# Kernel optimization log

Measured on AMD Instinct MI355X. Metric: run time of the kernel, lower is better.

## Reference

```python
import jax, jax.numpy as jnp
import numpy as np

B, S, CL = 64, 250, 16
WV, CV, FV, LAB = 50000, 100, 10, 20
WD, CD, CH, FD, HD = 300, 300, 50, 5, 200
T = LAB + 2          # CRF lattice size (labels + START + STOP)
START, STOP = LAB, LAB + 1
H = HD // 2          # hidden per LSTM direction
IN = CH + WD + FD    # 355


def _lstm_dir(x, m, w_ih, w_hh, b):
    # x: [B,S,IN], m: [B,S] bool -> masked unidirectional LSTM (PyTorch gate order i,f,g,o)
    Bn = x.shape[0]
    def step(carry, inp):
        h, c = carry
        xt, mt = inp
        g = xt @ w_ih.T + h @ w_hh.T + b
        i, f, gg, o = jnp.split(g, 4, axis=-1)
        c_new = jax.nn.sigmoid(f) * c + jax.nn.sigmoid(i) * jnp.tanh(gg)
        h_new = jax.nn.sigmoid(o) * jnp.tanh(c_new)
        mt = mt[:, None]
        h = jnp.where(mt, h_new, h)
        c = jnp.where(mt, c_new, c)
        return (h, c), h
    init = (jnp.zeros((Bn, H), x.dtype), jnp.zeros((Bn, H), x.dtype))
    _, hs = jax.lax.scan(step, init, (x.transpose(1, 0, 2), m.T))
    return hs.transpose(1, 0, 2)  # [B,S,H]


def _viterbi(feats, mask, trans):
    # feats: [B,S,T], mask: [B,S] bool, trans: [T,T] (trans[i,j] = score i->j)
    Bn = feats.shape[0]
    delta0 = trans[START][None, :] + feats[:, 0]  # [B,T]
    ident = jnp.arange(T)[None, :]
    def step(delta, inp):
        f_t, m_t = inp                              # [B,T], [B]
        sc = delta[:, :, None] + trans[None]        # [B,T(prev),T(cur)]
        vmax = sc.max(axis=1)
        bp = sc.argmax(axis=1)                      # [B,T]
        m = m_t[:, None]
        delta = jnp.where(m, vmax + f_t, delta)
        bp = jnp.where(m, bp, ident)                # pads: pass-through pointer
        return delta, bp
    delta, bps = jax.lax.scan(step, delta0,
                              (feats[:, 1:].transpose(1, 0, 2), mask[:, 1:].T))
    final = delta + trans[:, STOP][None, :]
    score = final.max(axis=1)                       # [B]
    last = final.argmax(axis=1)                     # [B]
    ar = jnp.arange(Bn)
    def back(tag, bp):
        prev = bp[ar, tag]
        return prev, prev
    _, prevs = jax.lax.scan(back, last, bps, reverse=True)  # [S-1,B]
    tag_seq = jnp.concatenate([prevs.transpose(1, 0), last[:, None]], axis=1)  # [B,S]
    return score, tag_seq


def setup_inputs() -> dict:
    key = jax.random.key(0)
    ks = jax.random.split(key, 20)
    lens = jax.random.randint(ks[0], (B,), S // 2, S + 1)
    mask = (jnp.arange(S)[None, :] < lens[:, None])
    def u(k, shape, scale):
        return jax.random.uniform(k, shape, jnp.float32, -scale, scale)
    return {
        "batch_word": jax.random.randint(ks[1], (B, S), 0, WV),
        "batch_features": jax.random.randint(ks[2], (B, S), 0, FV),
        "batch_wordlen": lens,
        "batch_char": jax.random.randint(ks[3], (B * S, CL), 0, CV),
        "batch_charlen": jax.random.randint(ks[4], (B * S,), 1, CL + 1),
        "batch_charrecover": jnp.arange(B * S),
        "mask": mask,
        "char_emb": u(ks[5], (CV, CD), np.sqrt(3.0 / CD)),
        "word_emb": u(ks[6], (WV, WD), np.sqrt(3.0 / WD)),
        "feat_emb": u(ks[7], (FV, FD), np.sqrt(3.0 / FD)),
        "conv_w": 0.1 * jax.random.normal(ks[8], (CH, CD, 3), jnp.float32),
        "conv_b": jnp.zeros((CH,), jnp.float32),
        "w_ih_f": 0.1 * jax.random.normal(ks[9], (4 * H, IN), jnp.float32),
        "w_hh_f": 0.1 * jax.random.normal(ks[10], (4 * H, H), jnp.float32),
        "b_f": jnp.zeros((4 * H,), jnp.float32),
        "w_ih_b": 0.1 * jax.random.normal(ks[11], (4 * H, IN), jnp.float32),
        "w_hh_b": 0.1 * jax.random.normal(ks[12], (4 * H, H), jnp.float32),
        "b_b": jnp.zeros((4 * H,), jnp.float32),
        "proj_w": 0.1 * jax.random.normal(ks[13], (HD, T), jnp.float32),
        "proj_b": jnp.zeros((T,), jnp.float32),
        "trans": 0.1 * jax.random.normal(ks[14], (T, T), jnp.float32),
    }


def reference(batch_word, batch_features, batch_wordlen, batch_char, batch_charlen,
              batch_charrecover, mask, char_emb, word_emb, feat_emb, conv_w, conv_b,
              w_ih_f, w_hh_f, b_f, w_ih_b, w_hh_b, b_b, proj_w, proj_b, trans):
    # char CNN: embed -> conv1d(k=3, pad=1) -> global max-pool (dropout: eval mode, identity)
    ce = char_emb[batch_char]                          # [B*S, CL, CD]
    conv = jax.lax.conv_general_dilated(
        ce.transpose(0, 2, 1), conv_w, window_strides=(1,), padding=[(1, 1)],
        dimension_numbers=('NCH', 'OIH', 'NCH')) + conv_b[None, :, None]
    char_feat = conv.max(axis=2)                       # [B*S, CH]
    char_feat = char_feat[batch_charrecover].reshape(B, S, CH)
    word_rep = jnp.concatenate(
        [word_emb[batch_word], char_feat, feat_emb[batch_features]], axis=2)  # [B,S,IN]
    # masked BiLSTM (equivalent to pack_padded_sequence: pads never update state)
    h_f = _lstm_dir(word_rep, mask, w_ih_f, w_hh_f, b_f)
    h_b = _lstm_dir(word_rep[:, ::-1], mask[:, ::-1], w_ih_b, w_hh_b, b_b)[:, ::-1]
    lstm_out = jnp.concatenate([h_f, h_b], axis=2)     # [B,S,HD]
    feats = lstm_out @ proj_w + proj_b                 # [B,S,T]
    score, tag_seq = _viterbi(feats, mask, trans)
    return tag_seq
```

## Files before the change

### kernel.cpp

```cpp
#include <hip/hip_runtime.h>
#include <hip/hip_bf16.h>
#include <math.h>

#define WS_U        0
#define WS_WPAD     15360
#define WS_WREP     359424
#define WS_PRE      6503424
#define WS_LSTM     359424
#define WS_FEATS    3559424

__global__ __launch_bounds__(256) void prepw_kernel(
    const float* __restrict__ wf, const float* __restrict__ wb,
    float* __restrict__ w_pad) {
  int idx = blockIdx.x * 256 + threadIdx.x;
  if (idx >= 896 * 384) return;
  int col = idx % 384, row = idx / 384;
  float v = 0.f;
  if (col < 355) {
    if (row < 400)      v = wf[row * 355 + col];
    else if (row < 800) v = wb[(row - 400) * 355 + col];
  }
  w_pad[idx] = v;
}

__global__ __launch_bounds__(256) void u_kernel(
    const float* __restrict__ char_emb, const float* __restrict__ conv_w,
    float* __restrict__ U) {
  int idx = blockIdx.x * 256 + threadIdx.x;
  if (idx >= 15000) return;
  int c = idx / 150, rem = idx % 150, k = rem / 50, o = rem % 50;
  float acc = 0.f;
  for (int i = 0; i < 300; i++)
    acc += char_emb[c * 300 + i] * conv_w[(o * 300 + i) * 3 + k];
  U[idx] = acc;
}

__global__ __launch_bounds__(64) void assemble_kernel(
    const int* __restrict__ batch_word, const int* __restrict__ batch_feats,
    const int* __restrict__ batch_char, const int* __restrict__ recover,
    const float* __restrict__ word_emb, const float* __restrict__ feat_emb,
    const float* __restrict__ conv_b, const float* __restrict__ U,
    float* __restrict__ wrep) {
  int n = blockIdx.x;
  int tid = threadIdx.x;
  __shared__ int ch[16];
  if (tid < 16) ch[tid] = batch_char[(size_t)recover[n] * 16 + tid];
  __syncthreads();
  float* dst = wrep + (size_t)n * 384;
  int w = batch_word[n];
  for (int i = tid; i < 300; i += 64) dst[i] = word_emb[(size_t)w * 300 + i];
  if (tid < 34) {
    int i = 350 + tid;
    dst[i] = (i < 355) ? feat_emb[batch_feats[n] * 5 + (i - 350)] : 0.f;
  }
  if (tid < 50) {
    int o = tid;
    float bo = conv_b[o];
    float m = -1e30f;
#pragma unroll
    for (int l = 0; l < 16; l++) {
      float v = bo + U[(ch[l] * 3 + 1) * 50 + o];
      if (l > 0)  v += U[(ch[l - 1] * 3 + 0) * 50 + o];
      if (l < 15) v += U[(ch[l + 1] * 3 + 2) * 50 + o];
      m = fmaxf(m, v);
    }
    dst[300 + o] = m;
  }
}

__global__ __launch_bounds__(256, 4) void gemm_kernel(
    const float* __restrict__ A, const float* __restrict__ B,
    float* __restrict__ C, const float* __restrict__ bf,
    const float* __restrict__ bb) {
  __shared__ float As[16][128];
  __shared__ float Bs[16][128];
  int tid = threadIdx.x;
  int m0 = blockIdx.x * 128;
  int n0 = blockIdx.y * 128;
  int tx = tid & 15, ty = tid >> 4;
  int lr = tid >> 2;
  int lc = (tid & 3) * 4;
  float acc[8][8];
#pragma unroll
  for (int i = 0; i < 8; i++)
#pragma unroll
    for (int j = 0; j < 8; j++) acc[i][j] = 0.f;

  for (int k0 = 0; k0 < 384; k0 += 16) {
#pragma unroll
    for (int h = 0; h < 2; h++) {
      int row = lr + h * 64;
      float4 av = *(const float4*)(A + (size_t)(m0 + row) * 384 + k0 + lc);
      As[lc + 0][row] = av.x; As[lc + 1][row] = av.y;
      As[lc + 2][row] = av.z; As[lc + 3][row] = av.w;
      float4 bv = *(const float4*)(B + (size_t)(n0 + row) * 384 + k0 + lc);
      Bs[lc + 0][row] = bv.x; Bs[lc + 1][row] = bv.y;
      Bs[lc + 2][row] = bv.z; Bs[lc + 3][row] = bv.w;
    }
    __syncthreads();
#pragma unroll
    for (int k = 0; k < 16; k++) {
      float a[8], b[8];
      *(float4*)&a[0] = *(const float4*)&As[k][ty * 8];
      *(float4*)&a[4] = *(const float4*)&As[k][ty * 8 + 4];
      *(float4*)&b[0] = *(const float4*)&Bs[k][tx * 8];
      *(float4*)&b[4] = *(const float4*)&Bs[k][tx * 8 + 4];
#pragma unroll
      for (int i = 0; i < 8; i++)
#pragma unroll
        for (int j = 0; j < 8; j++) acc[i][j] += a[i] * b[j];
    }
    __syncthreads();
  }
#pragma unroll
  for (int i = 0; i < 8; i++) {
    int m = m0 + ty * 8 + i;
#pragma unroll
    for (int jj = 0; jj < 8; jj++) {
      int j = n0 + tx * 8 + jj;
      if (j < 800) {
        float bias = (j < 400) ? bf[j] : bb[j - 400];
        C[(size_t)m * 800 + j] = acc[i][jj] + bias;
      }
    }
  }
}

__global__ __launch_bounds__(256, 1) void lstm_kernel(
    const float* __restrict__ pre, const float* __restrict__ w_hh_f,
    const float* __restrict__ w_hh_b, const int* __restrict__ wordlen,
    float* __restrict__ lstm_out) {
  int t = threadIdx.x;
  int dir = blockIdx.x >> 6;
  int r = blockIdx.x & 63;
  int len = wordlen[r];
  const float* __restrict__ Wh = dir ? w_hh_b : w_hh_f;
  __shared__ __align__(16) float h0[112];
  __shared__ __align__(16) float h1[112];

  const int j = t >> 1;
  const int odd = t & 1;
  const int rA = odd * 100 + j;
  const int rB = rA + 200;
  float4 WA[25], WB[25];
  if (t < 200) {
    const float4* wa = (const float4*)(Wh + (size_t)rA * 100);
    const float4* wb = (const float4*)(Wh + (size_t)rB * 100);
#pragma unroll
    for (int q = 0; q < 25; q++) { WA[q] = wa[q]; WB[q] = wb[q]; }
  }
  if (t < 112) { h0[t] = 0.f; h1[t] = 0.f; }

  float c_reg = 0.f, h_reg = 0.f;
  const float* __restrict__ pr = pre + dir * 400;
  const int p0 = dir ? 249 : 0;
  const int dp = dir ? -1 : 1;
  const size_t rowbase = (size_t)r * 250;
  const int j1 = rA;
  const int j2 = rB;

  float pvA1 = 0.f, pvA2 = 0.f, pvB1 = 0.f, pvB2 = 0.f;
  if (t < 200) {
    size_t offA = (rowbase + (size_t)p0) * 800;
    pvA1 = pr[offA + j1]; pvA2 = pr[offA + j2];
    size_t offB = (rowbase + (size_t)(p0 + dp)) * 800;
    pvB1 = pr[offB + j1]; pvB2 = pr[offB + j2];
  }
  __syncthreads();

#define LSTM_STEP(I, HRD, HWR, V1, V2)                                         \
  do {                                                                         \
    const int p = p0 + dp * (I);                                               \
    const bool valid = (p < len);                    \
    float g1 = 0.f, g2 = 0.f;                                                  \
    if (valid && t < 200) {                                                    \
      g1 = V1; g2 = V2;                                                        \
      _Pragma("unroll")                                                        \
      for (int q = 0; q < 25; q++) {                                           \
        float4 hv = *(const float4*)&(HRD)[4 * q];                             \
        g1 += hv.x * WA[q].x + hv.y * WA[q].y + hv.z * WA[q].z +               \
              hv.w * WA[q].w;                                                  \
        g2 += hv.x * WB[q].x + hv.y * WB[q].y + hv.z * WB[q].z +               \
              hv.w * WB[q].w;                                                  \
      }                                                                        \
    }                                                                          \
    if (t < 200) {              \
      const int ip = ((I) + 2 < 250) ? (I) + 2 : (I);                          \
      const size_t offp = (rowbase + (size_t)(p0 + dp * ip)) * 800;            \
      V1 = pr[offp + j1];                                                      \
      V2 = pr[offp + j2];                                                      \
    }                                                                          \
    if (valid) {                                                               \
      const float gi_in = __shfl_xor(g1, 1, 64);   \
      const float gg_in = __shfl_xor(g2, 1, 64);   \
      if (t < 200 && odd) {                                                    \
        const float si = 1.f / (1.f + expf(-gi_in));                           \
        const float sf = 1.f / (1.f + expf(-g1));                              \
        const float so = 1.f / (1.f + expf(-g2));                              \
        c_reg = sf * c_reg + si * tanhf(gg_in);                                \
        h_reg = so * tanhf(c_reg);                                             \
        (HWR)[j] = h_reg;                                                      \
        lstm_out[(rowbase + (size_t)p) * 200 + dir * 100 + j] = h_reg;         \
      }                                                                        \
         \
      asm volatile("s_waitcnt lgkmcnt(0)" ::: "memory");                       \
      __builtin_amdgcn_s_barrier();                                           \
    } else if (t < 200 && odd) {                                               \
                  \
      lstm_out[(rowbase + (size_t)p) * 200 + dir * 100 + j] = h_reg;           \
    }                                                                          \
  } while (0)

#pragma unroll 1
  for (int ii = 0; ii < 250; ii += 2) {
    LSTM_STEP(ii,     h0, h1, pvA1, pvA2);
    LSTM_STEP(ii + 1, h1, h0, pvB1, pvB2);
  }
#undef LSTM_STEP
}

__global__ __launch_bounds__(256) void proj_kernel(
    const float* __restrict__ lstm_out, const float* __restrict__ proj_w,
    const float* __restrict__ proj_b, float* __restrict__ feats) {
  __shared__ float L[8][200];
  int tid = threadIdx.x;
  size_t base = (size_t)blockIdx.x * 8 * 200;
  for (int idx = tid; idx < 1600; idx += 256)
    L[idx / 200][idx % 200] = lstm_out[base + idx];
  __syncthreads();
  int ty = tid >> 5, c = tid & 31;
  if (c < 22) {
    float acc = proj_b[c];
#pragma unroll 8
    for (int k = 0; k < 200; k++) acc += L[ty][k] * proj_w[k * 22 + c];
    feats[((size_t)blockIdx.x * 8 + ty) * 22 + c] = acc;
  }
}

__global__ __launch_bounds__(64) void viterbi_kernel(
    const float* __restrict__ feats, const float* __restrict__ trans,
    const int* __restrict__ wordlen, int* __restrict__ out) {
  int r = blockIdx.x;
  int lane = threadIdx.x;
  __shared__ float dsh[22];
  __shared__ float tsh[22][23];
  __shared__ unsigned char bps[250][22];
  int len = wordlen[r];
  const float* __restrict__ fr = feats + (size_t)r * 250 * 22;
  for (int idx = lane; idx < 484; idx += 64)
    tsh[idx / 22][idx % 22] = trans[idx];
  if (lane < 22) dsh[lane] = trans[20 * 22 + lane] + fr[lane];
  __syncthreads();
  for (int t = 1; t < 250; t++) {
    float best = -1e30f, fv = 0.f;
    int arg = 0;
    if (lane < 22) {
      fv = fr[t * 22 + lane];
#pragma unroll
      for (int k = 0; k < 22; k++) {
        float cand = dsh[k] + tsh[k][lane];
        if (cand > best) { best = cand; arg = k; }
      }
    }
    __syncthreads();
    if (lane < 22) {
      bool valid = t < len;
      if (valid) dsh[lane] = best + fv;
      bps[t][lane] = valid ? (unsigned char)arg : (unsigned char)lane;
    }
    __syncthreads();
  }
  if (lane == 0) {
    float best = -1e30f;
    int last = 0;
#pragma unroll
    for (int k = 0; k < 22; k++) {
      float cand = dsh[k] + tsh[k][21];
      if (cand > best) { best = cand; last = k; }
    }
    int tag = last;
    out[r * 250 + 249] = tag;
    for (int t = 249; t >= 1; t--) {
      tag = bps[t][tag];
      out[r * 250 + t - 1] = tag;
    }
  }
}

extern "C" void kernel_launch(void* const* d_in, const int* in_sizes, int n_in,
                              void* d_out, int out_size, void* d_ws, size_t ws_size,
                              hipStream_t stream) {
  const int* batch_word  = (const int*)d_in[0];
  const int* batch_feats = (const int*)d_in[1];
  const int* wordlen     = (const int*)d_in[2];
  const int* batch_char  = (const int*)d_in[3];
  const int* recover     = (const int*)d_in[5];
  const float* char_emb  = (const float*)d_in[7];
  const float* word_emb  = (const float*)d_in[8];
  const float* feat_emb  = (const float*)d_in[9];
  const float* conv_w    = (const float*)d_in[10];
  const float* conv_b    = (const float*)d_in[11];
  const float* w_ih_f    = (const float*)d_in[12];
  const float* w_hh_f    = (const float*)d_in[13];
  const float* b_f       = (const float*)d_in[14];
  const float* w_ih_b    = (const float*)d_in[15];
  const float* w_hh_b    = (const float*)d_in[16];
  const float* b_b       = (const float*)d_in[17];
  const float* proj_w    = (const float*)d_in[18];
  const float* proj_b    = (const float*)d_in[19];
  const float* trans     = (const float*)d_in[20];
  int* out = (int*)d_out;
  float* ws = (float*)d_ws;

  float* U        = ws + WS_U;
  float* w_pad    = ws + WS_WPAD;
  float* wrep     = ws + WS_WREP;
  float* pre      = ws + WS_PRE;
  float* lstm_out = ws + WS_LSTM;
  float* feats    = ws + WS_FEATS;

  prepw_kernel<<<1344, 256, 0, stream>>>(w_ih_f, w_ih_b, w_pad);
  u_kernel<<<59, 256, 0, stream>>>(char_emb, conv_w, U);
  assemble_kernel<<<16000, 64, 0, stream>>>(batch_word, batch_feats, batch_char,
                                            recover, word_emb, feat_emb, conv_b,
                                            U, wrep);
  dim3 ggrid(125, 7);
  gemm_kernel<<<ggrid, 256, 0, stream>>>(wrep, w_pad, pre, b_f, b_b);
  lstm_kernel<<<128, 256, 0, stream>>>(pre, w_hh_f, w_hh_b, wordlen, lstm_out);
  proj_kernel<<<2000, 256, 0, stream>>>(lstm_out, proj_w, proj_b, feats);
  viterbi_kernel<<<64, 64, 0, stream>>>(feats, trans, wordlen, out);
}
```

Measured before the change: 809.7 us.

## Split LSTM recurrence into one gate row per thread with readlane broadcast of h

The recurrent LSTM kernel now uses 448 threads per block with four threads per hidden unit, one per gate. Each thread holds a single row of W_hh instead of two. Each wave loads a chunk of h from shared memory and broadcasts it with readlane instead of having every thread read all of h from LDS. Gate values are gathered with three xor-shuffles, and the raw barrier is replaced by a full __syncthreads every step. The aim is to halve the serial dot-product length per step. In exchange it adds more waves per barrier and scalar readlane traffic.

```diff
diff --git a/kernel.cpp b/kernel.cpp
--- a/kernel.cpp
+++ b/kernel.cpp
@@ -126,11 +126,12 @@
   }
 }
 
-__global__ __launch_bounds__(256, 1) void lstm_kernel(
+__global__ __launch_bounds__(448) void lstm_kernel(
     const float* __restrict__ pre, const float* __restrict__ w_hh_f,
     const float* __restrict__ w_hh_b, const int* __restrict__ wordlen,
     float* __restrict__ lstm_out) {
   int t = threadIdx.x;
+  int lane = t & 63;
   int dir = blockIdx.x >> 6;
   int r = blockIdx.x & 63;
   int len = wordlen[r];
@@ -138,16 +139,19 @@
   __shared__ __align__(16) float h0[112];
   __shared__ __align__(16) float h1[112];
 
-  const int j = t >> 1;
-  const int odd = t & 1;
-  const int rA = odd * 100 + j;
-  const int rB = rA + 200;
-  float4 WA[25], WB[25];
-  if (t < 200) {
-    const float4* wa = (const float4*)(Wh + (size_t)rA * 100);
-    const float4* wb = (const float4*)(Wh + (size_t)rB * 100);
-#pragma unroll
-    for (int q = 0; q < 25; q++) { WA[q] = wa[q]; WB[q] = wb[q]; }
+  const int v = t >> 2;
+  const int s = t & 3;
+  const int row = s * 100 + v;
+  const bool act = (v < 100);
+
+  float4 W[25];
+  if (act) {
+    const float4* wr = (const float4*)(Wh + (size_t)row * 100);
+#pragma unroll
+    for (int q = 0; q < 25; q++) W[q] = wr[q];
+  } else {
+#pragma unroll
+    for (int q = 0; q < 25; q++) W[q] = make_float4(0.f, 0.f, 0.f, 0.f);
   }
   if (t < 112) { h0[t] = 0.f; h1[t] = 0.f; }
 
@@ -156,67 +160,65 @@
   const int p0 = dir ? 249 : 0;
   const int dp = dir ? -1 : 1;
   const size_t rowbase = (size_t)r * 250;
-  const int j1 = rA;
-  const int j2 = rB;
-
-  float pvA1 = 0.f, pvA2 = 0.f, pvB1 = 0.f, pvB2 = 0.f;
-  if (t < 200) {
-    size_t offA = (rowbase + (size_t)p0) * 800;
-    pvA1 = pr[offA + j1]; pvA2 = pr[offA + j2];
-    size_t offB = (rowbase + (size_t)(p0 + dp)) * 800;
-    pvB1 = pr[offB + j1]; pvB2 = pr[offB + j2];
-  }
+
+  float pvA = 0.f, pvB = 0.f;
+  if (act) {
+    pvA = pr[(rowbase + (size_t)p0) * 800 + row];
+    pvB = pr[(rowbase + (size_t)(p0 + dp)) * 800 + row];
+  }
+  const int cl = (lane < 25) ? lane : 0;
   __syncthreads();
 
-#define LSTM_STEP(I, HRD, HWR, V1, V2)                                         \
+#define RL(x, q) __uint_as_float(__builtin_amdgcn_readlane(__float_as_uint(x), (q)))
+
+#define LSTM_STEP(I, HRD, HWR, PV)                                             \
   do {                                                                         \
     const int p = p0 + dp * (I);                                               \
-    const bool valid = (p < len);                    \
-    float g1 = 0.f, g2 = 0.f;                                                  \
-    if (valid && t < 200) {                                                    \
-      g1 = V1; g2 = V2;                                                        \
+    const bool valid = (p < len);                           \
+    float g = 0.f;                                                             \
+    if (valid) {                                                               \
+      float4 hch = *(const float4*)&(HRD)[4 * cl];                             \
+      g = PV;                                                                  \
       _Pragma("unroll")                                                        \
       for (int q = 0; q < 25; q++) {                                           \
-        float4 hv = *(const float4*)&(HRD)[4 * q];                             \
-        g1 += hv.x * WA[q].x + hv.y * WA[q].y + hv.z * WA[q].z +               \
-              hv.w * WA[q].w;                                                  \
-        g2 += hv.x * WB[q].x + hv.y * WB[q].y + hv.z * WB[q].z +               \
-              hv.w * WB[q].w;                                                  \
+        const float hx = RL(hch.x, q);                                         \
+        const float hy = RL(hch.y, q);                                         \
+        const float hz = RL(hch.z, q);                                         \
+        const float hw = RL(hch.w, q);                                         \
+        g += hx * W[q].x + hy * W[q].y + hz * W[q].z + hw * W[q].w;            \
       }                                                                        \
     }                                                                          \
-    if (t < 200) {              \
+    if (act) {                  \
       const int ip = ((I) + 2 < 250) ? (I) + 2 : (I);                          \
-      const size_t offp = (rowbase + (size_t)(p0 + dp * ip)) * 800;            \
-      V1 = pr[offp + j1];                                                      \
-      V2 = pr[offp + j2];                                                      \
+      PV = pr[(rowbase + (size_t)(p0 + dp * ip)) * 800 + row];                 \
     }                                                                          \
     if (valid) {                                                               \
-      const float gi_in = __shfl_xor(g1, 1, 64);   \
-      const float gg_in = __shfl_xor(g2, 1, 64);   \
-      if (t < 200 && odd) {                                                    \
-        const float si = 1.f / (1.f + expf(-gi_in));                           \
-        const float sf = 1.f / (1.f + expf(-g1));                              \
-        const float so = 1.f / (1.f + expf(-g2));                              \
+      const float gf_in = __shfl_xor(g, 1, 64);       \
+      const float gg_in = __shfl_xor(g, 2, 64);       \
+      const float go_in = __shfl_xor(g, 3, 64);       \
+      if (act && s == 0) {                                                     \
+        const float si = 1.f / (1.f + expf(-g));                               \
+        const float sf = 1.f / (1.f + expf(-gf_in));                           \
+        const float so = 1.f / (1.f + expf(-go_in));                           \
         c_reg = sf * c_reg + si * tanhf(gg_in);                                \
         h_reg = so * tanhf(c_reg);                                             \
-        (HWR)[j] = h_reg;                                                      \
-        lstm_out[(rowbase + (size_t)p) * 200 + dir * 100 + j] = h_reg;         \
+        (HWR)[v] = h_reg;                                                      \
+        lstm_out[(rowbase + (size_t)p) * 200 + dir * 100 + v] = h_reg;         \
       }                                                                        \
-         \
-      asm volatile("s_waitcnt lgkmcnt(0)" ::: "memory");                       \
-      __builtin_amdgcn_s_barrier();                                           \
-    } else if (t < 200 && odd) {                                               \
-                  \
-      lstm_out[(rowbase + (size_t)p) * 200 + dir * 100 + j] = h_reg;           \
+    } else if (act && s == 0) {                                                \
+        \
+      lstm_out[(rowbase + (size_t)p) * 200 + dir * 100 + v] = h_reg;           \
     }                                                                          \
+    __syncthreads();                   \
   } while (0)
 
 #pragma unroll 1
   for (int ii = 0; ii < 250; ii += 2) {
-    LSTM_STEP(ii,     h0, h1, pvA1, pvA2);
-    LSTM_STEP(ii + 1, h1, h0, pvB1, pvB2);
+    LSTM_STEP(ii,     h0, h1, pvA);
+    LSTM_STEP(ii + 1, h1, h0, pvB);
   }
 #undef LSTM_STEP
+#undef RL
 }
 
 __global__ __launch_bounds__(256) void proj_kernel(
@@ -326,7 +328,7 @@
                                             U, wrep);
   dim3 ggrid(125, 7);
   gemm_kernel<<<ggrid, 256, 0, stream>>>(wrep, w_pad, pre, b_f, b_b);
-  lstm_kernel<<<128, 256, 0, stream>>>(pre, w_hh_f, w_hh_b, wordlen, lstm_out);
+  lstm_kernel<<<128, 448, 0, stream>>>(pre, w_hh_f, w_hh_b, wordlen, lstm_out);
   proj_kernel<<<2000, 256, 0, stream>>>(lstm_out, proj_w, proj_b, feats);
   viterbi_kernel<<<64, 64, 0, stream>>>(feats, trans, wordlen, out);
 }
```

After: 847.6 us. 4.7% more time.
